# Kernel optimization log

Hardware: AMD Instinct MI355X
Metric: run time of the kernel (lower is better)

The kernel has to match this reference:

```python
import jax, jax.numpy as jnp
import numpy as np

B, S, D, H, FF = 4, 2048, 512, 8, 2048
HD = D // H
WINDOW = 64  # local attention half-window in rank space
EPS = 1e-5


def _layer_norm(v, g, b):
    m = jnp.mean(v, axis=-1, keepdims=True)
    var = jnp.mean(jnp.square(v - m), axis=-1, keepdims=True)
    return (v - m) / jnp.sqrt(var + EPS) * g + b


def setup_inputs() -> dict:
    key = jax.random.key(0)
    ks = jax.random.split(key, 10)
    sc = 0.02
    x = jax.random.normal(ks[0], (B, S, D), jnp.float32)
    padding_mask = jnp.zeros((B, S), dtype=bool)
    i = jnp.arange(S)
    local = jnp.abs(i[:, None] - i[None, :]) <= WINDOW
    glob = (i[:, None] == 0) | (i[None, :] == 0)  # global spectrum token at pos 0
    attn_mask = jnp.where(local | glob, 0.0, -jnp.inf).astype(jnp.float32)
    return {
        "x": x,
        "padding_mask": padding_mask,
        "attn_mask": attn_mask,
        "in_proj_w": jax.random.normal(ks[1], (3 * D, D), jnp.float32) * sc,
        "in_proj_b": jnp.zeros((3 * D,), jnp.float32),
        "out_proj_w": jax.random.normal(ks[2], (D, D), jnp.float32) * sc,
        "out_proj_b": jnp.zeros((D,), jnp.float32),
        "ln1_g": jnp.ones((D,), jnp.float32),
        "ln1_b": jnp.zeros((D,), jnp.float32),
        "ln2_g": jnp.ones((D,), jnp.float32),
        "ln2_b": jnp.zeros((D,), jnp.float32),
        "ff_w1": jax.random.normal(ks[3], (FF, D), jnp.float32) * sc,
        "ff_b1": jnp.zeros((FF,), jnp.float32),
        "ff_w2": jax.random.normal(ks[4], (D, FF), jnp.float32) * sc,
        "ff_b2": jnp.zeros((D,), jnp.float32),
    }


def reference(x, padding_mask, attn_mask, in_proj_w, in_proj_b, out_proj_w,
              out_proj_b, ln1_g, ln1_b, ln2_g, ln2_b, ff_w1, ff_b1, ff_w2, ff_b2):
    # pre-LN attention
    a = _layer_norm(x, ln1_g, ln1_b)
    qkv = a @ in_proj_w.T + in_proj_b  # [B,S,3D]
    q, k, v = jnp.split(qkv, 3, axis=-1)
    to_heads = lambda t: t.reshape(B, S, H, HD).transpose(0, 2, 1, 3)
    q, k, v = to_heads(q), to_heads(k), to_heads(v)
    scores = jnp.einsum('bhqd,bhkd->bhqk', q, k) * (HD ** -0.5)
    # float attn_mask path: key_padding_mask converted to additive -inf floats
    kpm = jnp.where(padding_mask, -jnp.inf, 0.0).astype(scores.dtype)
    scores = scores + attn_mask[None, None, :, :] + kpm[:, None, None, :]
    p = jax.nn.softmax(scores, axis=-1)
    o = jnp.einsum('bhqk,bhkd->bhqd', p, v).transpose(0, 2, 1, 3).reshape(B, S, D)
    o = o @ out_proj_w.T + out_proj_b
    x = x + o  # residual (dropout = 0)
    # pre-LN feed-forward with exact GELU (torch nn.GELU default)
    f = _layer_norm(x, ln2_g, ln2_b)
    f = jax.nn.gelu(f @ ff_w1.T + ff_b1, approximate=False) @ ff_w2.T + ff_b2
    return x + f
```

## Files before the change

kernel.cpp:

```cpp
#include <hip/hip_runtime.h>
#include <hip/hip_bf16.h>
#include <math.h>

namespace {

constexpr int kB = 4, kS = 2048, kD = 512, kH = 8, kFF = 2048;
constexpr int kM = kB * kS;
constexpr int kHD = kD / kH;
constexpr int kWin = 64;

typedef __attribute__((ext_vector_type(8))) short short8;
typedef __attribute__((ext_vector_type(4))) float f32x4;

__device__ __forceinline__ float bf2f(__hip_bfloat16 v) { return __bfloat162float(v); }
__device__ __forceinline__ __hip_bfloat16 f2bf(float v) { return __float2bfloat16(v); }
__device__ __forceinline__ int iclamp(int v, int lo, int hi) { return v < lo ? lo : (v > hi ? hi : v); }

__device__ __forceinline__ void async16(const void* g, void* l) {
  __builtin_amdgcn_global_load_lds((const __attribute__((address_space(1))) void*)g,
                                   (__attribute__((address_space(3))) void*)l, 16, 0, 0);
}

__global__ void cast_f32_bf16(const float* __restrict__ s, __hip_bfloat16* __restrict__ d, int n) {
  int i = (blockIdx.x * blockDim.x + threadIdx.x) * 4;
  if (i >= n) return;
  float4 v = *(const float4*)(s + i);
  union { __hip_bfloat16 h[4]; uint2 u; } t;
  t.h[0] = f2bf(v.x); t.h[1] = f2bf(v.y); t.h[2] = f2bf(v.z); t.h[3] = f2bf(v.w);
  *(uint2*)(d + i) = t.u;
}

__global__ __launch_bounds__(64)
void ln_rows(const float* __restrict__ x, const float* __restrict__ g,
             const float* __restrict__ bta, __hip_bfloat16* __restrict__ out) {
  int row = blockIdx.x;
  int lane = threadIdx.x;
  const float* xr = x + (size_t)row * kD;
  int c = lane * 8;
  float4 v0 = *(const float4*)(xr + c);
  float4 v1 = *(const float4*)(xr + c + 4);
  float s  = v0.x + v0.y + v0.z + v0.w + v1.x + v1.y + v1.z + v1.w;
  float ss = v0.x*v0.x + v0.y*v0.y + v0.z*v0.z + v0.w*v0.w
           + v1.x*v1.x + v1.y*v1.y + v1.z*v1.z + v1.w*v1.w;
#pragma unroll
  for (int o = 32; o > 0; o >>= 1) { s += __shfl_xor(s, o); ss += __shfl_xor(ss, o); }
  float mean = s * (1.0f / kD);
  float inv  = rsqrtf(ss * (1.0f / kD) - mean * mean + 1e-5f);
  float4 g0 = *(const float4*)(g + c),   g1 = *(const float4*)(g + c + 4);
  float4 b0 = *(const float4*)(bta + c), b1 = *(const float4*)(bta + c + 4);
  union { __hip_bfloat16 h[8]; int4 u; } t;
  t.h[0] = f2bf((v0.x - mean) * inv * g0.x + b0.x);
  t.h[1] = f2bf((v0.y - mean) * inv * g0.y + b0.y);
  t.h[2] = f2bf((v0.z - mean) * inv * g0.z + b0.z);
  t.h[3] = f2bf((v0.w - mean) * inv * g0.w + b0.w);
  t.h[4] = f2bf((v1.x - mean) * inv * g1.x + b1.x);
  t.h[5] = f2bf((v1.y - mean) * inv * g1.y + b1.y);
  t.h[6] = f2bf((v1.z - mean) * inv * g1.z + b1.z);
  t.h[7] = f2bf((v1.w - mean) * inv * g1.w + b1.w);
  *(int4*)(out + (size_t)row * kD + c) = t.u;
}

__global__ __launch_bounds__(64)
void attn_tile(const __hip_bfloat16* __restrict__ qkv, __hip_bfloat16* __restrict__ o) {
  const int bh = blockIdx.x;
  const int tq = blockIdx.y;
  const int b = bh >> 3, h = bh & 7;
  const int lane = threadIdx.x;
  const int quad = lane >> 4, col = lane & 15;
  const int q0 = tq * 16;
  const int kbase = q0 - kWin;

  __shared__ __hip_bfloat16 Pt[160 * 20];

  const __hip_bfloat16* base = qkv + (size_t)b * kS * (3 * kD);

  short8 aq0, aq1;
  {
    const __hip_bfloat16* qrow = base + (size_t)(q0 + col) * (3 * kD) + h * kHD + quad * 8;
    aq0 = *(const short8*)qrow;
    aq1 = *(const short8*)(qrow + 32);
  }

  f32x4 sc[10];
#pragma unroll
  for (int t = 0; t < 10; ++t) {
    int krow = (t < 9) ? iclamp(kbase + t * 16 + col, 0, kS - 1) : col;
    const short8* kp = (const short8*)(base + (size_t)krow * (3 * kD) + kD + h * kHD + quad * 8);
    f32x4 a = (f32x4){0.f, 0.f, 0.f, 0.f};
    a = __builtin_amdgcn_mfma_f32_16x16x32_bf16(aq0, kp[0], a, 0, 0, 0);
    a = __builtin_amdgcn_mfma_f32_16x16x32_bf16(aq1, kp[4], a, 0, 0, 0);
    sc[t] = a;
  }

  float rowmax[4] = {-1e30f, -1e30f, -1e30f, -1e30f};
#pragma unroll
  for (int t = 0; t < 10; ++t) {
#pragma unroll
    for (int r = 0; r < 4; ++r) {
      int q = q0 + quad * 4 + r;
      bool valid;
      if (t < 9) {
        int k = kbase + t * 16 + col;
        valid = (k >= 0) && (k < kS) && ((q - k <= kWin && k - q <= kWin) || k == 0);
      } else {
        valid = (col == 0) && (kbase > 0);
      }
      float s = valid ? sc[t][r] * 0.125f : -1e30f;
      sc[t][r] = s;
      rowmax[r] = fmaxf(rowmax[r], s);
    }
  }
#pragma unroll
  for (int r = 0; r < 4; ++r)
#pragma unroll
    for (int off = 1; off < 16; off <<= 1)
      rowmax[r] = fmaxf(rowmax[r], __shfl_xor(rowmax[r], off));

  float rowsum[4] = {0.f, 0.f, 0.f, 0.f};
#pragma unroll
  for (int t = 0; t < 10; ++t)
#pragma unroll
    for (int r = 0; r < 4; ++r) {
      float e = __expf(sc[t][r] - rowmax[r]);
      sc[t][r] = e;
      rowsum[r] += e;
    }
#pragma unroll
  for (int r = 0; r < 4; ++r)
#pragma unroll
    for (int off = 1; off < 16; off <<= 1)
      rowsum[r] += __shfl_xor(rowsum[r], off);

#pragma unroll
  for (int t = 0; t < 10; ++t) {
    union { ushort u[4]; unsigned long long ll; } pk;
#pragma unroll
    for (int r = 0; r < 4; ++r) {
      __hip_bfloat16 hv = f2bf(sc[t][r]);
      pk.u[r] = *(ushort*)&hv;
    }
    *(unsigned long long*)&Pt[(t * 16 + col) * 20 + quad * 4] = pk.ll;
  }
  __syncthreads();

  f32x4 oacc[4];
#pragma unroll
  for (int n = 0; n < 4; ++n) oacc[n] = (f32x4){0.f, 0.f, 0.f, 0.f};

#pragma unroll
  for (int c = 0; c < 5; ++c) {
    union { short s[8]; short8 v; } pa;
    const __hip_bfloat16* vrow[8];
#pragma unroll
    for (int j = 0; j < 8; ++j) {
      int kidx = c * 32 + quad * 8 + j;
      pa.s[j] = *(const short*)&Pt[kidx * 20 + col];
      int key = (kidx < 144) ? iclamp(kbase + kidx, 0, kS - 1) : (kidx - 144);
      vrow[j] = base + (size_t)key * (3 * kD) + 2 * kD + h * kHD;
    }
#pragma unroll
    for (int n = 0; n < 4; ++n) {
      union { short s[8]; short8 v; } vb;
#pragma unroll
      for (int j = 0; j < 8; ++j) vb.s[j] = *(const short*)(vrow[j] + n * 16 + col);
      oacc[n] = __builtin_amdgcn_mfma_f32_16x16x32_bf16(pa.v, vb.v, oacc[n], 0, 0, 0);
    }
  }

#pragma unroll
  for (int n = 0; n < 4; ++n)
#pragma unroll
    for (int r = 0; r < 4; ++r) {
      int q = q0 + quad * 4 + r;
      o[(size_t)(b * kS + q) * kD + h * kHD + n * 16 + col] = f2bf(oacc[n][r] / rowsum[r]);
    }
}

__global__ __launch_bounds__(1024)
void attn_q0(const __hip_bfloat16* __restrict__ qkv, __hip_bfloat16* __restrict__ o) {
  const int b = blockIdx.x >> 3, h = blockIdx.x & 7;
  const int t = threadIdx.x;
  const int lane = t & 63, wid = t >> 6;
  __shared__ float qs[kHD];
  __shared__ float sc[kS];
  __shared__ float redm[16];
  __shared__ float reds[16];
  __shared__ float part[16][kHD];

  const __hip_bfloat16* base = qkv + (size_t)b * kS * (3 * kD);
  if (t < kHD) qs[t] = bf2f(base[h * kHD + t]) * 0.125f;
  __syncthreads();

  float m = -1e30f;
#pragma unroll
  for (int it = 0; it < 2; ++it) {
    int k = t + it * 1024;
    const short8* kp = (const short8*)(base + (size_t)k * (3 * kD) + kD + h * kHD);
    float s = 0.f;
#pragma unroll
    for (int cc = 0; cc < 8; ++cc) {
      union { short8 v; __hip_bfloat16 hh[8]; } u;
      u.v = kp[cc];
#pragma unroll
      for (int d = 0; d < 8; ++d) s += qs[cc * 8 + d] * bf2f(u.hh[d]);
    }
    sc[k] = s;
    m = fmaxf(m, s);
  }
#pragma unroll
  for (int off = 32; off > 0; off >>= 1) m = fmaxf(m, __shfl_xor(m, off));
  if (lane == 0) redm[wid] = m;
  __syncthreads();
  float M = redm[0];
#pragma unroll
  for (int i = 1; i < 16; ++i) M = fmaxf(M, redm[i]);

  float ls = 0.f;
#pragma unroll
  for (int it = 0; it < 2; ++it) {
    int k = t + it * 1024;
    float e = __expf(sc[k] - M);
    sc[k] = e;
    ls += e;
  }
#pragma unroll
  for (int off = 32; off > 0; off >>= 1) ls += __shfl_xor(ls, off);
  if (lane == 0) reds[wid] = ls;
  __syncthreads();
  float L = 0.f;
#pragma unroll
  for (int i = 0; i < 16; ++i) L += reds[i];

  float a = 0.f;
  const int d = lane;
#pragma unroll 8
  for (int kk = 0; kk < 128; ++kk) {
    int k = wid * 128 + kk;
    a += sc[k] * bf2f(base[(size_t)k * (3 * kD) + 2 * kD + h * kHD + d]);
  }
  part[wid][d] = a;
  __syncthreads();
  if (t < kHD) {
    float s = 0.f;
#pragma unroll
    for (int c = 0; c < 16; ++c) s += part[c][t];
    o[(size_t)(b * kS) * kD + h * kHD + t] = f2bf(s / L);
  }
}

template <int TN, int EPI, typename OT>
__global__ __launch_bounds__(256, 2)
void gemm_bt(const __hip_bfloat16* __restrict__ A, const __hip_bfloat16* __restrict__ W,
             const float* __restrict__ bias, const float* __restrict__ resid,
             OT* __restrict__ C, int Ndim, int K) {
  constexpr int NF = TN / 32;
  __shared__ __hip_bfloat16 As[128 * 64];
  __shared__ __hip_bfloat16 Ws[TN * 64];

  const int tid = threadIdx.x;
  const int lane = tid & 63, w = tid >> 6;
  const int wm = w >> 1, wn = w & 1;
  const int quad = lane >> 4, mrow = lane & 15;
  const int m0 = blockIdx.y * 128, n0 = blockIdx.x * TN;

  const int lrow = lane >> 3;
  const int lcol = ((lane & 7) ^ lrow) << 3;

  f32x4 acc[4][NF];
#pragma unroll
  for (int i = 0; i < 4; ++i)
#pragma unroll
    for (int j = 0; j < NF; ++j) acc[i][j] = (f32x4){0.f, 0.f, 0.f, 0.f};

  for (int kt = 0; kt < K; kt += 64) {
#pragma unroll
    for (int it = 0; it < 4; ++it) {
      int c = w * 4 + it;
      async16(A + (size_t)(m0 + c * 8 + lrow) * K + kt + lcol, &As[c * 512]);
    }
#pragma unroll
    for (int it = 0; it < NF; ++it) {
      int c = w * NF + it;
      async16(W + (size_t)(n0 + c * 8 + lrow) * K + kt + lcol, &Ws[c * 512]);
    }
    __syncthreads();
#pragma unroll
    for (int kk = 0; kk < 64; kk += 32) {
      const int ch = (kk >> 3) + quad;
      const int sw = (ch ^ (mrow & 7)) << 3;
      short8 af[4], wf[NF];
#pragma unroll
      for (int i = 0; i < 4; ++i)
        af[i] = *(const short8*)&As[(wm * 64 + i * 16 + mrow) * 64 + sw];
#pragma unroll
      for (int j = 0; j < NF; ++j)
        wf[j] = *(const short8*)&Ws[(wn * (TN / 2) + j * 16 + mrow) * 64 + sw];
#pragma unroll
      for (int i = 0; i < 4; ++i)
#pragma unroll
        for (int j = 0; j < NF; ++j)
          acc[i][j] = __builtin_amdgcn_mfma_f32_16x16x32_bf16(af[i], wf[j], acc[i][j], 0, 0, 0);
    }
    __syncthreads();
  }

#pragma unroll
  for (int i = 0; i < 4; ++i) {
#pragma unroll
    for (int r = 0; r < 4; ++r) {
      int row = m0 + wm * 64 + i * 16 + quad * 4 + r;
#pragma unroll
      for (int j = 0; j < NF; ++j) {
        int col = n0 + wn * (TN / 2) + j * 16 + mrow;
        float v = acc[i][j][r] + bias[col];
        if (EPI == 1) v = 0.5f * v * (1.0f + erff(v * 0.70710678118f));
        if (EPI == 2) v += resid[(size_t)row * Ndim + col];
        if constexpr (__is_same(OT, float)) C[(size_t)row * Ndim + col] = v;
        else                                C[(size_t)row * Ndim + col] = f2bf(v);
      }
    }
  }
}

}

extern "C" void kernel_launch(void* const* d_in, const int* in_sizes, int n_in,
                              void* d_out, int out_size, void* d_ws, size_t ws_size,
                              hipStream_t stream) {
  const float* x          = (const float*)d_in[0];
  const float* in_proj_w  = (const float*)d_in[3];
  const float* in_proj_b  = (const float*)d_in[4];
  const float* out_proj_w = (const float*)d_in[5];
  const float* out_proj_b = (const float*)d_in[6];
  const float* ln1_g      = (const float*)d_in[7];
  const float* ln1_b      = (const float*)d_in[8];
  const float* ln2_g      = (const float*)d_in[9];
  const float* ln2_b      = (const float*)d_in[10];
  const float* ff_w1      = (const float*)d_in[11];
  const float* ff_b1      = (const float*)d_in[12];
  const float* ff_w2      = (const float*)d_in[13];
  const float* ff_b2      = (const float*)d_in[14];
  float* out = (float*)d_out;

  char* ws = (char*)d_ws;
  size_t off = 0;
  auto carve = [&](size_t bytes) { char* p = ws + off; off += (bytes + 255) & ~(size_t)255; return p; };
  __hip_bfloat16* wqkv_bf = (__hip_bfloat16*)carve((size_t)3 * kD * kD * 2);
  __hip_bfloat16* wout_bf = (__hip_bfloat16*)carve((size_t)kD * kD * 2);
  __hip_bfloat16* wff1_bf = (__hip_bfloat16*)carve((size_t)kFF * kD * 2);
  __hip_bfloat16* wff2_bf = (__hip_bfloat16*)carve((size_t)kD * kFF * 2);
  __hip_bfloat16* a_bf    = (__hip_bfloat16*)carve((size_t)kM * kD * 2);
  __hip_bfloat16* qkv_bf  = (__hip_bfloat16*)carve((size_t)kM * 3 * kD * 2);
  __hip_bfloat16* o_bf    = (__hip_bfloat16*)carve((size_t)kM * kD * 2);
  float*          r1      = (float*)carve((size_t)kM * kD * 4);
  __hip_bfloat16* ln2_bf  = (__hip_bfloat16*)carve((size_t)kM * kD * 2);
  __hip_bfloat16* ff1_bf  = (__hip_bfloat16*)carve((size_t)kM * kFF * 2);

  {
    int n;
    n = 3 * kD * kD; cast_f32_bf16<<<(n / 4 + 255) / 256, 256, 0, stream>>>(in_proj_w, wqkv_bf, n);
    n = kD * kD;     cast_f32_bf16<<<(n / 4 + 255) / 256, 256, 0, stream>>>(out_proj_w, wout_bf, n);
    n = kFF * kD;    cast_f32_bf16<<<(n / 4 + 255) / 256, 256, 0, stream>>>(ff_w1, wff1_bf, n);
    n = kD * kFF;    cast_f32_bf16<<<(n / 4 + 255) / 256, 256, 0, stream>>>(ff_w2, wff2_bf, n);
  }

  ln_rows<<<kM, 64, 0, stream>>>(x, ln1_g, ln1_b, a_bf);
  gemm_bt<128, 0, __hip_bfloat16><<<dim3(1536 / 128, kM / 128), 256, 0, stream>>>(
      a_bf, wqkv_bf, in_proj_b, nullptr, qkv_bf, 3 * kD, kD);
  attn_tile<<<dim3(kB * kH, kS / 16), 64, 0, stream>>>(qkv_bf, o_bf);
  attn_q0<<<kB * kH, 1024, 0, stream>>>(qkv_bf, o_bf);
  gemm_bt<64, 2, float><<<dim3(kD / 64, kM / 128), 256, 0, stream>>>(
      o_bf, wout_bf, out_proj_b, x, r1, kD, kD);
  ln_rows<<<kM, 64, 0, stream>>>(r1, ln2_g, ln2_b, ln2_bf);
  gemm_bt<128, 1, __hip_bfloat16><<<dim3(kFF / 128, kM / 128), 256, 0, stream>>>(
      ln2_bf, wff1_bf, ff_b1, nullptr, ff1_bf, kFF, kD);
  gemm_bt<64, 2, float><<<dim3(kD / 64, kM / 128), 256, 0, stream>>>(
      ff1_bf, wff2_bf, ff_b2, r1, out, kD, kFF);
}
```

Baseline: 267.5 us.

## Transpose V for vectorized attention loads and swizzle GEMM block order

Adds a kernel that writes V transposed per batch and head into a reused workspace buffer. The attention PV step can then load each B-operand as one 16-byte vector instead of eight scalar strided loads. The GEMMs switch to a 1D grid with a grouped M-block ordering to improve L2 reuse, and launch bounds are raised to allow more resident blocks. The cost is an extra kernel launch and an extra pass over V; the clamp to kS-8 at the sequence edges also changes which keys are read there, so edge correctness depends on the masking.

```diff
diff --git a/kernel.cpp b/kernel.cpp
--- a/kernel.cpp
+++ b/kernel.cpp
@@ -61,7 +61,36 @@
 }
 
 __global__ __launch_bounds__(64)
-void attn_tile(const __hip_bfloat16* __restrict__ qkv, __hip_bfloat16* __restrict__ o) {
+void transpose_v(const __hip_bfloat16* __restrict__ qkv, __hip_bfloat16* __restrict__ vt) {
+  const int id = blockIdx.x;
+  const int st = id & 31, h = (id >> 5) & 7, b = id >> 8;
+  const int lane = threadIdx.x;
+  __shared__ __hip_bfloat16 Ls[64 * 68];
+  const int r8 = lane >> 3, c8 = (lane & 7) << 3;
+  const __hip_bfloat16* src = qkv + (size_t)(b * kS + st * 64) * (3 * kD) + 2 * kD + h * kHD;
+#pragma unroll
+  for (int i = 0; i < 8; ++i) {
+    int row = i * 8 + r8;
+    union { int4 v; uint2 d2[2]; } u;
+    u.v = *(const int4*)(src + (size_t)row * (3 * kD) + c8);
+    *(uint2*)&Ls[row * 68 + c8] = u.d2[0];
+    *(uint2*)&Ls[row * 68 + c8 + 4] = u.d2[1];
+  }
+  __syncthreads();
+  __hip_bfloat16* dst = vt + (size_t)(b * kH + h) * kHD * kS + st * 64;
+#pragma unroll
+  for (int i = 0; i < 8; ++i) {
+    int d = i * 8 + r8;
+    union { __hip_bfloat16 hh[8]; int4 v; } u;
+#pragma unroll
+    for (int j = 0; j < 8; ++j) u.hh[j] = Ls[(c8 + j) * 68 + d];
+    *(int4*)(dst + (size_t)d * kS + c8) = u.v;
+  }
+}
+
+__global__ __launch_bounds__(64)
+void attn_tile(const __hip_bfloat16* __restrict__ qkv, const __hip_bfloat16* __restrict__ vt,
+               __hip_bfloat16* __restrict__ o) {
   const int bh = blockIdx.x;
   const int tq = blockIdx.y;
   const int b = bh >> 3, h = bh & 7;
@@ -73,6 +102,7 @@
   __shared__ __hip_bfloat16 Pt[160 * 20];
 
   const __hip_bfloat16* base = qkv + (size_t)b * kS * (3 * kD);
+  const __hip_bfloat16* vt_bh = vt + (size_t)(b * kH + h) * kHD * kS;
 
   short8 aq0, aq1;
   {
@@ -150,20 +180,14 @@
 #pragma unroll
   for (int c = 0; c < 5; ++c) {
     union { short s[8]; short8 v; } pa;
-    const __hip_bfloat16* vrow[8];
-#pragma unroll
-    for (int j = 0; j < 8; ++j) {
-      int kidx = c * 32 + quad * 8 + j;
-      pa.s[j] = *(const short*)&Pt[kidx * 20 + col];
-      int key = (kidx < 144) ? iclamp(kbase + kidx, 0, kS - 1) : (kidx - 144);
-      vrow[j] = base + (size_t)key * (3 * kD) + 2 * kD + h * kHD;
-    }
+#pragma unroll
+    for (int j = 0; j < 8; ++j) pa.s[j] = *(const short*)&Pt[(c * 32 + quad * 8 + j) * 20 + col];
+    const int kc = c * 32 + quad * 8;
+    const int kstart = (kc < 144) ? iclamp(kbase + kc, 0, kS - 8) : (kc - 144);
 #pragma unroll
     for (int n = 0; n < 4; ++n) {
-      union { short s[8]; short8 v; } vb;
-#pragma unroll
-      for (int j = 0; j < 8; ++j) vb.s[j] = *(const short*)(vrow[j] + n * 16 + col);
-      oacc[n] = __builtin_amdgcn_mfma_f32_16x16x32_bf16(pa.v, vb.v, oacc[n], 0, 0, 0);
+      short8 vb = *(const short8*)(vt_bh + (size_t)(n * 16 + col) * kS + kstart);
+      oacc[n] = __builtin_amdgcn_mfma_f32_16x16x32_bf16(pa.v, vb, oacc[n], 0, 0, 0);
     }
   }
 
@@ -248,8 +272,8 @@
   }
 }
 
-template <int TN, int EPI, typename OT>
-__global__ __launch_bounds__(256, 2)
+template <int TN, int NB, int EPI, typename OT>
+__global__ __launch_bounds__(256, (TN == 64) ? 4 : 3)
 void gemm_bt(const __hip_bfloat16* __restrict__ A, const __hip_bfloat16* __restrict__ W,
              const float* __restrict__ bias, const float* __restrict__ resid,
              OT* __restrict__ C, int Ndim, int K) {
@@ -257,11 +281,15 @@
   __shared__ __hip_bfloat16 As[128 * 64];
   __shared__ __hip_bfloat16 Ws[TN * 64];
 
+  const int id = blockIdx.x;
+  const int rr = id & 7, tt = id >> 3;
+  const int nb = tt % NB, mb = (tt / NB) * 8 + rr;
+
   const int tid = threadIdx.x;
   const int lane = tid & 63, w = tid >> 6;
   const int wm = w >> 1, wn = w & 1;
   const int quad = lane >> 4, mrow = lane & 15;
-  const int m0 = blockIdx.y * 128, n0 = blockIdx.x * TN;
+  const int m0 = mb * 128, n0 = nb * TN;
 
   const int lrow = lane >> 3;
   const int lcol = ((lane & 7) ^ lrow) << 3;
@@ -355,6 +383,7 @@
   float*          r1      = (float*)carve((size_t)kM * kD * 4);
   __hip_bfloat16* ln2_bf  = (__hip_bfloat16*)carve((size_t)kM * kD * 2);
   __hip_bfloat16* ff1_bf  = (__hip_bfloat16*)carve((size_t)kM * kFF * 2);
+  __hip_bfloat16* vt      = a_bf;
 
   {
     int n;
@@ -365,15 +394,16 @@
   }
 
   ln_rows<<<kM, 64, 0, stream>>>(x, ln1_g, ln1_b, a_bf);
-  gemm_bt<128, 0, __hip_bfloat16><<<dim3(1536 / 128, kM / 128), 256, 0, stream>>>(
+  gemm_bt<128, 12, 0, __hip_bfloat16><<<64 * 12, 256, 0, stream>>>(
       a_bf, wqkv_bf, in_proj_b, nullptr, qkv_bf, 3 * kD, kD);
-  attn_tile<<<dim3(kB * kH, kS / 16), 64, 0, stream>>>(qkv_bf, o_bf);
+  transpose_v<<<kB * kH * 32, 64, 0, stream>>>(qkv_bf, vt);
+  attn_tile<<<dim3(kB * kH, kS / 16), 64, 0, stream>>>(qkv_bf, vt, o_bf);
   attn_q0<<<kB * kH, 1024, 0, stream>>>(qkv_bf, o_bf);
-  gemm_bt<64, 2, float><<<dim3(kD / 64, kM / 128), 256, 0, stream>>>(
+  gemm_bt<64, 8, 2, float><<<64 * 8, 256, 0, stream>>>(
       o_bf, wout_bf, out_proj_b, x, r1, kD, kD);
   ln_rows<<<kM, 64, 0, stream>>>(r1, ln2_g, ln2_b, ln2_bf);
-  gemm_bt<128, 1, __hip_bfloat16><<<dim3(kFF / 128, kM / 128), 256, 0, stream>>>(
+  gemm_bt<128, 16, 1, __hip_bfloat16><<<64 * 16, 256, 0, stream>>>(
       ln2_bf, wff1_bf, ff_b1, nullptr, ff1_bf, kFF, kD);
-  gemm_bt<64, 2, float><<<dim3(kD / 64, kM / 128), 256, 0, stream>>>(
+  gemm_bt<64, 8, 2, float><<<64 * 8, 256, 0, stream>>>(
       ff1_bf, wff2_bf, ff_b2, r1, out, kD, kFF);
 }
```

Result: faster. 253.5 us (-5.2%).
